# Kernel optimization log

Measured on AMD Instinct MI355X. Metric: run time of the kernel, lower is better.

The kernel has to match this reference:

```python
import jax, jax.numpy as jnp
import numpy as np

N_SIN = 3  # fcn_n_sin (static)


def setup_inputs() -> dict:
    key = jax.random.key(0)
    ks = jax.random.split(key, 5)
    B, I, O, H = 256, 128, 128, 32
    F = 1 + 2 * N_SIN
    return {
        "x": jax.random.normal(ks[0], (B, I), dtype=jnp.float32),
        "W1": jax.random.normal(ks[1], (I, O, H, F), dtype=jnp.float32) * 0.3,
        "W2": jax.random.normal(ks[2], (I, O, 1, H), dtype=jnp.float32) * 0.3,
        "B1": jax.random.normal(ks[3], (I, O, H), dtype=jnp.float32) * 0.1,
        "B2": jax.random.normal(ks[4], (I, O, 1), dtype=jnp.float32) * 0.1,
    }


def reference(x, W1, W2, B1, B2):
    # x: [B, I]; per-(i,o) edge MLP on a scalar input, summed over i.
    omega = (2.0 ** jnp.arange(N_SIN)).astype(x.dtype)          # [S]
    ox = x[..., None] * omega                                    # [B, I, S]
    feat = jnp.concatenate([x[..., None], jnp.sin(ox), jnp.cos(ox)], axis=-1)  # [B, I, 1+2S]
    # First linear: per-edge [F -> H]
    h = jnp.einsum('bif,iohf->bioh', feat, W1) + B1              # [B, I, O, H]
    h = jax.nn.silu(h)
    # Second linear: per-edge [H -> 1], then sum over input dims i
    out = jnp.einsum('bioh,ioh->bio', h, W2[:, :, 0, :]) + B2[:, :, 0]  # [B, I, O]
    return out.sum(axis=1)                                       # [B, O]
```

## Files before the change

### kernel.cpp

```cpp
#include <hip/hip_runtime.h>
#include <hip/hip_bf16.h>

#define B_DIM 256
#define I_DIM 128
#define O_DIM 128
#define H_DIM 32
#define F_DIM 7
#define ICHUNK 4
#define NCHUNK (I_DIM / ICHUNK)

typedef __attribute__((ext_vector_type(8))) short short8;
typedef __attribute__((ext_vector_type(4))) float float4v;

__device__ inline short bf16s(float v) {
    union { __hip_bfloat16 h; short s; } u;
    u.h = __float2bfloat16(v);
    return u.s;
}

template <bool USE_WS>
__global__ __launch_bounds__(256, 4)
void fcnkan_mfma(const float* __restrict__ x,
                 const float* __restrict__ W1,
                 const float* __restrict__ W2,
                 const float* __restrict__ B1,
                 const float* __restrict__ B2,
                 float* __restrict__ ws,
                 float* __restrict__ out) {
    __shared__ __align__(16) short feat_s[ICHUNK * B_DIM * 8];
    __shared__ __align__(16) short w1_s[ICHUNK * H_DIM * 8];
    __shared__ float b1_s[ICHUNK * H_DIM];
    __shared__ float w2_s[ICHUNK * H_DIM];

    const int tid  = threadIdx.x;
    const int o    = blockIdx.x;
    const int ic0  = blockIdx.y * ICHUNK;
    const int w    = tid >> 6;
    const int lane = tid & 63;
    const int m    = lane & 15;
    const int q    = lane >> 4;

    const short8 zero8 = {};

    {
        const float4* xp = reinterpret_cast<const float4*>(x + (size_t)tid * I_DIM + ic0);
        float4 x0 = xp[0];
        float xr[4] = {x0.x, x0.y, x0.z, x0.w};
        #pragma unroll
        for (int il = 0; il < ICHUNK; ++il) {
            float xv = xr[il];
            float s1 = __sinf(xv), c1 = __cosf(xv);
            float s2 = 2.f * s1 * c1, c2 = 1.f - 2.f * s1 * s1;
            float s4 = 2.f * s2 * c2, c4 = 1.f - 2.f * s2 * s2;
            short8 a;
            a[0] = bf16s(xv); a[1] = bf16s(s1); a[2] = bf16s(s2); a[3] = bf16s(s4);
            a[4] = bf16s(c1); a[5] = bf16s(c2); a[6] = bf16s(c4); a[7] = 0;
            *reinterpret_cast<short8*>(feat_s + (il * B_DIM + tid) * 8) = a;
        }
    }
    if (tid < ICHUNK * H_DIM) {
        int il = tid >> 5, h = tid & 31;
        size_t iobase = (size_t)(ic0 + il) * O_DIM + o;
        const float* wr = W1 + iobase * (H_DIM * F_DIM) + h * F_DIM;
        short8 bfr;
        #pragma unroll
        for (int f = 0; f < F_DIM; ++f) bfr[f] = bf16s(wr[f]);
        bfr[7] = 0;
        *reinterpret_cast<short8*>(w1_s + tid * 8) = bfr;
        b1_s[tid] = B1[iobase * H_DIM + h];
        w2_s[tid] = W2[iobase * H_DIM + h];
    }
    __syncthreads();

    float acc[16];
    #pragma unroll
    for (int r = 0; r < 16; ++r) acc[r] = 0.f;

    #pragma unroll 1
    for (int il = 0; il < ICHUNK; ++il) {
        const short8* fS = reinterpret_cast<const short8*>(feat_s) + il * B_DIM;
        const short8* wS = reinterpret_cast<const short8*>(w1_s) + il * H_DIM;

        short8 afrag[4];
        #pragma unroll
        for (int t = 0; t < 4; ++t)
            afrag[t] = fS[w * 64 + t * 16 + m];

        short8 bfrag[2];
        float  b1v[2], w2v[2];
        #pragma unroll
        for (int nt = 0; nt < 2; ++nt) {
            int h = nt * 16 + m;
            short8 b = wS[h];
            bfrag[nt] = (q == 0) ? b : zero8;
            b1v[nt] = b1_s[il * H_DIM + h];
            w2v[nt] = w2_s[il * H_DIM + h];
        }

        #pragma unroll
        for (int nt = 0; nt < 2; ++nt) {
            float4v c0 = {b1v[nt], b1v[nt], b1v[nt], b1v[nt]};
            #pragma unroll
            for (int t = 0; t < 4; ++t) {
                float4v z = __builtin_amdgcn_mfma_f32_16x16x32_bf16(
                    afrag[t], bfrag[nt], c0, 0, 0, 0);
                #pragma unroll
                for (int r = 0; r < 4; ++r) {
                    float zz = z[r];
                    float sg = __builtin_amdgcn_rcpf(1.f + __expf(-zz));
                    acc[t * 4 + r] = fmaf(zz * sg, w2v[nt], acc[t * 4 + r]);
                }
            }
        }
    }

    #pragma unroll
    for (int r = 0; r < 16; ++r) {
        float v = acc[r];
        v += __shfl_xor(v, 1, 64);
        v += __shfl_xor(v, 2, 64);
        v += __shfl_xor(v, 4, 64);
        v += __shfl_xor(v, 8, 64);
        acc[r] = v;
    }

    float b2c = 0.f;
    #pragma unroll
    for (int il = 0; il < ICHUNK; ++il) b2c += B2[(size_t)(ic0 + il) * O_DIM + o];

    if (m == 0) {
        if (USE_WS) {
            float* wsp = ws + ((size_t)blockIdx.y * O_DIM + o) * B_DIM;
            #pragma unroll
            for (int t = 0; t < 4; ++t)
                #pragma unroll
                for (int r = 0; r < 4; ++r)
                    wsp[w * 64 + t * 16 + q * 4 + r] = acc[t * 4 + r] + b2c;
        } else {
            #pragma unroll
            for (int t = 0; t < 4; ++t)
                #pragma unroll
                for (int r = 0; r < 4; ++r) {
                    int b = w * 64 + t * 16 + q * 4 + r;
                    atomicAdd(&out[(size_t)b * O_DIM + o], acc[t * 4 + r] + b2c);
                }
        }
    }
}

__global__ __launch_bounds__(256)
void reduce_kernel(const float* __restrict__ ws, float* __restrict__ out) {
    const int o = blockIdx.x;
    const int b = threadIdx.x;
    float s = 0.f;
    #pragma unroll
    for (int c = 0; c < NCHUNK; ++c)
        s += ws[((size_t)c * O_DIM + o) * B_DIM + b];
    out[(size_t)b * O_DIM + o] = s;
}

extern "C" void kernel_launch(void* const* d_in, const int* in_sizes, int n_in,
                              void* d_out, int out_size, void* d_ws, size_t ws_size,
                              hipStream_t stream) {
    const float* x  = (const float*)d_in[0];
    const float* W1 = (const float*)d_in[1];
    const float* W2 = (const float*)d_in[2];
    const float* B1 = (const float*)d_in[3];
    const float* B2 = (const float*)d_in[4];
    float* out = (float*)d_out;
    float* ws  = (float*)d_ws;

    const size_t ws_need = (size_t)NCHUNK * O_DIM * B_DIM * sizeof(float);
    dim3 grid(O_DIM, NCHUNK);
    if (ws_size >= ws_need) {
        fcnkan_mfma<true><<<grid, 256, 0, stream>>>(x, W1, W2, B1, B2, ws, out);
        reduce_kernel<<<O_DIM, B_DIM, 0, stream>>>(ws, out);
    } else {
        hipMemsetAsync(out, 0, (size_t)out_size * sizeof(float), stream);
        fcnkan_mfma<false><<<grid, 256, 0, stream>>>(x, W1, W2, B1, B2, ws, out);
    }
}
```

Baseline: 107.8 us.

## Precompute features in a separate kernel and load W1 with coalesced accesses

A new kernel computes the bf16 sin/cos feature vectors once per (i,b) and stores them in workspace. The main kernel then copies them into LDS with direct global-to-LDS loads instead of recomputing the transcendentals in every block. W1 staging also changes from per-thread strided 7-float reads to a coalesced loop across all threads. This adds one kernel launch and a feature buffer write/read, and it relies on there being enough workspace for both buffers. The global-to-LDS copy is issued without an explicit wait before the barrier.

```diff
diff --git a/kernel.cpp b/kernel.cpp
--- a/kernel.cpp
+++ b/kernel.cpp
@@ -12,10 +12,27 @@
 typedef __attribute__((ext_vector_type(8))) short short8;
 typedef __attribute__((ext_vector_type(4))) float float4v;
 
+#define GLOAD_LDS16(g, l) __builtin_amdgcn_global_load_lds( \
+    (const __attribute__((address_space(1))) void*)(g),     \
+    (__attribute__((address_space(3))) void*)(l), 16, 0, 0)
+
 __device__ inline short bf16s(float v) {
     union { __hip_bfloat16 h; short s; } u;
     u.h = __float2bfloat16(v);
     return u.s;
+}
+
+__global__ void feat_kernel(const float* __restrict__ x, short* __restrict__ featw) {
+    const int i = blockIdx.x;
+    const int b = threadIdx.x;
+    float xv = x[(size_t)b * I_DIM + i];
+    float s1 = __sinf(xv), c1 = __cosf(xv);
+    float s2 = 2.f * s1 * c1, c2 = 1.f - 2.f * s1 * s1;
+    float s4 = 2.f * s2 * c2, c4 = 1.f - 2.f * s2 * s2;
+    short8 a;
+    a[0] = bf16s(xv); a[1] = bf16s(s1); a[2] = bf16s(s2); a[3] = bf16s(s4);
+    a[4] = bf16s(c1); a[5] = bf16s(c2); a[6] = bf16s(c4); a[7] = 0;
+    *reinterpret_cast<short8*>(featw + ((size_t)i * B_DIM + b) * 8) = a;
 }
 
 template <bool USE_WS>
@@ -25,6 +42,7 @@
                  const float* __restrict__ W2,
                  const float* __restrict__ B1,
                  const float* __restrict__ B2,
+                 const short* __restrict__ featw,
                  float* __restrict__ ws,
                  float* __restrict__ out) {
     __shared__ __align__(16) short feat_s[ICHUNK * B_DIM * 8];
@@ -42,7 +60,15 @@
 
     const short8 zero8 = {};
 
-    {
+    if (USE_WS) {
+        const char* src = reinterpret_cast<const char*>(featw + (size_t)ic0 * B_DIM * 8);
+        char* dst = reinterpret_cast<char*>(feat_s);
+        #pragma unroll
+        for (int t = 0; t < 4; ++t) {
+            int c = w * 4 + t;
+            GLOAD_LDS16(src + c * 1024 + lane * 16, dst + c * 1024 + lane * 16);
+        }
+    } else {
         const float4* xp = reinterpret_cast<const float4*>(x + (size_t)tid * I_DIM + ic0);
         float4 x0 = xp[0];
         float xr[4] = {x0.x, x0.y, x0.z, x0.w};
@@ -58,15 +84,18 @@
             *reinterpret_cast<short8*>(feat_s + (il * B_DIM + tid) * 8) = a;
         }
     }
+
+    for (int e = tid; e < ICHUNK * H_DIM * F_DIM; e += 256) {
+        int il = e / (H_DIM * F_DIM);
+        int r  = e - il * (H_DIM * F_DIM);
+        float v = W1[((size_t)(ic0 + il) * O_DIM + o) * (H_DIM * F_DIM) + r];
+        int h = r / F_DIM, f = r - h * F_DIM;
+        w1_s[(il * H_DIM + h) * 8 + f] = bf16s(v);
+    }
     if (tid < ICHUNK * H_DIM) {
+        w1_s[tid * 8 + 7] = 0;
         int il = tid >> 5, h = tid & 31;
         size_t iobase = (size_t)(ic0 + il) * O_DIM + o;
-        const float* wr = W1 + iobase * (H_DIM * F_DIM) + h * F_DIM;
-        short8 bfr;
-        #pragma unroll
-        for (int f = 0; f < F_DIM; ++f) bfr[f] = bf16s(wr[f]);
-        bfr[7] = 0;
-        *reinterpret_cast<short8*>(w1_s + tid * 8) = bfr;
         b1_s[tid] = B1[iobase * H_DIM + h];
         w2_s[tid] = W2[iobase * H_DIM + h];
     }
@@ -168,15 +197,19 @@
     const float* B1 = (const float*)d_in[3];
     const float* B2 = (const float*)d_in[4];
     float* out = (float*)d_out;
-    float* ws  = (float*)d_ws;
-
-    const size_t ws_need = (size_t)NCHUNK * O_DIM * B_DIM * sizeof(float);
+
+    const size_t feat_bytes = (size_t)I_DIM * B_DIM * 8 * sizeof(short);
+    const size_t part_bytes = (size_t)NCHUNK * O_DIM * B_DIM * sizeof(float);
+    short* featw = (short*)d_ws;
+    float* part  = (float*)((char*)d_ws + feat_bytes);
+
     dim3 grid(O_DIM, NCHUNK);
-    if (ws_size >= ws_need) {
-        fcnkan_mfma<true><<<grid, 256, 0, stream>>>(x, W1, W2, B1, B2, ws, out);
-        reduce_kernel<<<O_DIM, B_DIM, 0, stream>>>(ws, out);
+    if (ws_size >= feat_bytes + part_bytes) {
+        feat_kernel<<<I_DIM, B_DIM, 0, stream>>>(x, featw);
+        fcnkan_mfma<true><<<grid, 256, 0, stream>>>(x, W1, W2, B1, B2, featw, part, out);
+        reduce_kernel<<<O_DIM, B_DIM, 0, stream>>>(part, out);
     } else {
         hipMemsetAsync(out, 0, (size_t)out_size * sizeof(float), stream);
-        fcnkan_mfma<false><<<grid, 256, 0, stream>>>(x, W1, W2, B1, B2, ws, out);
-    }
-}
+        fcnkan_mfma<false><<<grid, 256, 0, stream>>>(x, W1, W2, B1, B2, featw, part, out);
+    }
+}
```

New measurement: 114.1 us. 5.8% more time.
